# Performance work log

Measured on AMD Instinct MI355X. Metric: run time of the kernel, lower is better.

Reference implementation:

```python
import jax, jax.numpy as jnp
import numpy as np

TEMPERATURE = 0.07
EPS = 1e-8

def setup_inputs() -> dict:
    key = jax.random.key(0)
    k1, k2 = jax.random.split(key)
    features = jax.random.normal(k1, (8192, 512), dtype=jnp.float32)
    labels = jax.random.randint(k2, (8192,), 0, 100, dtype=jnp.int64)
    return {"features": features, "labels": labels}

def reference(features, labels):
    # L2-normalize rows (torch F.normalize uses eps=1e-12 clamp on norm)
    norm = jnp.maximum(jnp.linalg.norm(features, axis=1, keepdims=True), 1e-12)
    f = features / norm                                   # [B, D]
    sim = jnp.matmul(f, f.T) / TEMPERATURE                # [B, B]
    B = features.shape[0]
    same_label = (labels[:, None] == labels[None, :]).astype(features.dtype)
    diag = jnp.eye(B, dtype=bool)
    mask = jnp.where(diag, 0.0, same_label)               # positives, diag removed
    exp_sim = jnp.where(diag, 0.0, jnp.exp(sim))          # diag zeroed
    positive_sum = jnp.sum(exp_sim * mask, axis=1)        # [B]
    negative_sum = jnp.sum(exp_sim * (1.0 - mask), axis=1)
    loss = -jnp.log(positive_sum / (positive_sum + negative_sum + EPS))
    return loss.mean()
```

## Files before the change

kernel.cpp:

```cpp
#include <hip/hip_runtime.h>

#define BATCH 8192
#define DIM   512
#define NBLK  2080

typedef __attribute__((ext_vector_type(2))) long long2_t;
typedef __attribute__((ext_vector_type(4))) float f32x4;
typedef unsigned char u8;

__device__ __forceinline__ void gload_lds16(const void* g, void* l){
  __builtin_amdgcn_global_load_lds(
      (const __attribute__((address_space(1))) void*)g,
      (__attribute__((address_space(3))) void*)l, 16, 0, 0);
}

template<int CTRL>
__device__ __forceinline__ float dpp_add(float v){
  int s = __builtin_amdgcn_update_dpp(0, __float_as_int(v), CTRL, 0xF, 0xF, true);
  return v + __int_as_float(s);
}
__device__ __forceinline__ float red16(float v){
  v = dpp_add<0xB1>(v);
  v = dpp_add<0x4E>(v);
  v = dpp_add<0x141>(v);
  v = dpp_add<0x140>(v);
  return v;
}

__device__ __forceinline__ u8 f2e4m3(float v){
  unsigned s = (__float_as_uint(v) >> 24) & 0x80u;
  float a = fabsf(v);
  if (a < 0.0009765625f) return (u8)s;
  if (a < 0.015625f){
    int qd = (int)rintf(a * 512.0f);
    return (u8)(s | (unsigned)qd);
  }
  unsigned u = __float_as_uint(a);
  int E = (int)(u >> 23) - 127;
  unsigned m = u & 0x7FFFFF;
  unsigned mant = m >> 20;
  unsigned rem  = m & 0xFFFFF;
  mant += (rem > 0x80000u || (rem == 0x80000u && (mant & 1u))) ? 1u : 0u;
  if (mant == 8u){ mant = 0u; E += 1; }
  return (u8)(s | ((unsigned)(E + 7) << 3) | mant);
}

__global__ __launch_bounds__(256) void k_normalize(const float* __restrict__ x,
                                                   u8* __restrict__ q){
  const int row  = blockIdx.x * 4 + (threadIdx.x >> 6);
  const int lane = threadIdx.x & 63;
  const float* xr = x + (size_t)row * DIM + lane * 8;
  float4 a = *(const float4*)xr;
  float4 b = *(const float4*)(xr + 4);
  float s = a.x*a.x + a.y*a.y + a.z*a.z + a.w*a.w
          + b.x*b.x + b.y*b.y + b.z*b.z + b.w*b.w;
  #pragma unroll
  for (int m = 1; m < 64; m <<= 1) s += __shfl_xor(s, m);
  const float inv = 1.0f / fmaxf(sqrtf(s), 1e-12f);
  float f[8] = {a.x, a.y, a.z, a.w, b.x, b.y, b.z, b.w};
  union { u8 b[8]; unsigned long long u; } pk;
  #pragma unroll
  for (int e = 0; e < 8; e++) pk.b[e] = f2e4m3(f[e] * inv);
  const int kb = lane >> 3;
  const int g  = lane & 7;
  const int sw = (row >> 1) & 3;
  const size_t off = (size_t)row * DIM + kb * 64
                   + (size_t)(((g & 3) ^ sw) * 16 + (g >> 2) * 8);
  *(unsigned long long*)(q + off) = pk.u;
}

__global__ __launch_bounds__(256, 3) void k_gemm(const u8* __restrict__ q,
                                                 const int* __restrict__ labels,
                                                 float* __restrict__ ppos,
                                                 float* __restrict__ ptot){
  __shared__ u8 sA[2][128 * 64];
  __shared__ u8 sB[2][128 * 64];
  __shared__ int labI[128], labJ[128];

  const int bid = (blockIdx.x & 7) * 260 + (blockIdx.x >> 3);
  int bj = (int)((sqrtf(8.0f * (float)bid + 1.0f) - 1.0f) * 0.5f);
  while ((bj + 1) * (bj + 2) / 2 <= bid) bj++;
  while (bj * (bj + 1) / 2 > bid) bj--;
  const int bi = bid - bj * (bj + 1) / 2;
  const bool mirror = (bi != bj);
  const int rowbase = bi * 128, colbase = bj * 128;

  const int t    = threadIdx.x;
  const int lane = t & 63;
  const int w    = t >> 6;
  const int wr   = w >> 1, wc = w & 1;
  const int lrow = lane & 15;
  const int g    = lane >> 4;

  if (t < 128) labI[t] = labels[rowbase + t];
  else         labJ[t - 128] = labels[colbase + (t - 128)];

  const int gs = (g ^ ((lrow >> 1) & 3)) * 16;
  int ra[4], rb[4];
  #pragma unroll
  for (int m = 0; m < 4; m++) ra[m] = (wr * 64 + m * 16 + lrow) * 64 + gs;
  #pragma unroll
  for (int n = 0; n < 4; n++) rb[n] = (wc * 64 + n * 16 + lrow) * 64 + gs;

  const u8* srcA = q + (size_t)(rowbase + (t >> 2)) * DIM + (t & 3) * 16;
  const u8* srcB = q + (size_t)(colbase + (t >> 2)) * DIM + (t & 3) * 16;
  const int dL = t * 16;

#define STAGE(BUF, KT) do{                                                \
    gload_lds16(srcA + (KT) * 64,             sA[BUF] + dL);              \
    gload_lds16(srcA + (KT) * 64 + 64 * DIM,  sA[BUF] + dL + 4096);       \
    gload_lds16(srcB + (KT) * 64,             sB[BUF] + dL);              \
    gload_lds16(srcB + (KT) * 64 + 64 * DIM,  sB[BUF] + dL + 4096);       \
  }while(0)

  f32x4 acc[4][4];
  #pragma unroll
  for (int m = 0; m < 4; m++)
    #pragma unroll
    for (int n = 0; n < 4; n++)
      acc[m][n] = (f32x4){0.f, 0.f, 0.f, 0.f};

  STAGE(0, 0);
  __syncthreads();

  for (int kt = 0; kt < 8; ++kt){
    const int cur = kt & 1;
    if (kt < 7) STAGE(cur ^ 1, kt + 1);
    const u8* pA = sA[cur];
    const u8* pB = sB[cur];
    long2_t av[4], bv[4];
    #pragma unroll
    for (int n = 0; n < 4; n++) bv[n] = *(const long2_t*)(pB + rb[n]);
    #pragma unroll
    for (int m = 0; m < 4; m++) av[m] = *(const long2_t*)(pA + ra[m]);
    #pragma unroll
    for (int m = 0; m < 4; m++)
      #pragma unroll
      for (int n = 0; n < 4; n++)
        acc[m][n] = __builtin_amdgcn_mfma_f32_16x16x32_fp8_fp8(
            av[m][0], bv[n][0], acc[m][n], 0, 0, 0);
    #pragma unroll
    for (int m = 0; m < 4; m++)
      #pragma unroll
      for (int n = 0; n < 4; n++)
        acc[m][n] = __builtin_amdgcn_mfma_f32_16x16x32_fp8_fp8(
            av[m][1], bv[n][1], acc[m][n], 0, 0, 0);
    __syncthreads();
  }
#undef STAGE

  const int i0 = rowbase + wr * 64;
  const int j0 = colbase + wc * 64;

  int li_[4][4], lj_[4];
  #pragma unroll
  for (int m = 0; m < 4; m++)
    #pragma unroll
    for (int e = 0; e < 4; e++)
      li_[m][e] = labI[wr * 64 + m * 16 + g * 4 + e];
  #pragma unroll
  for (int n = 0; n < 4; n++)
    lj_[n] = labJ[wc * 64 + n * 16 + lrow];

  const float invT = 14.285714285714286f;
  #pragma unroll
  for (int m = 0; m < 4; m++)
    #pragma unroll
    for (int n = 0; n < 4; n++)
      #pragma unroll
      for (int e = 0; e < 4; e++){
        int i = i0 + m * 16 + g * 4 + e;
        int j = j0 + n * 16 + lrow;
        acc[m][n][e] = (i == j) ? 0.0f : __expf(acc[m][n][e] * invT);
      }

  {
    float* pp = ppos + (size_t)(2 * bj + wc) * BATCH;
    float* pt = ptot + (size_t)(2 * bj + wc) * BATCH;
    #pragma unroll
    for (int m = 0; m < 4; m++){
      float tr[4] = {0, 0, 0, 0}, pr[4] = {0, 0, 0, 0};
      #pragma unroll
      for (int n = 0; n < 4; n++){
        int lj = lj_[n];
        #pragma unroll
        for (int e = 0; e < 4; e++){
          float v = acc[m][n][e];
          tr[e] += v;
          pr[e] += (li_[m][e] == lj) ? v : 0.0f;
        }
      }
      #pragma unroll
      for (int e = 0; e < 4; e++){
        tr[e] = red16(tr[e]);
        pr[e] = red16(pr[e]);
      }
      if (lrow == 0){
        int ib = i0 + m * 16 + g * 4;
        #pragma unroll
        for (int e = 0; e < 4; e++){
          pt[ib + e] = tr[e];
          pp[ib + e] = pr[e];
        }
      }
    }
  }

  if (mirror){
    float* pp = ppos + (size_t)(2 * bi + wr) * BATCH;
    float* pt = ptot + (size_t)(2 * bi + wr) * BATCH;
    #pragma unroll
    for (int n = 0; n < 4; n++){
      float ts = 0.f, ps = 0.f;
      int lj = lj_[n];
      #pragma unroll
      for (int m = 0; m < 4; m++)
        #pragma unroll
        for (int e = 0; e < 4; e++){
          float v = acc[m][n][e];
          ts += v;
          ps += (li_[m][e] == lj) ? v : 0.0f;
        }
      ts += __shfl_xor(ts, 16); ps += __shfl_xor(ps, 16);
      ts += __shfl_xor(ts, 32); ps += __shfl_xor(ps, 32);
      if (lane < 16){
        int j = j0 + n * 16 + lane;
        pt[j] = ts;
        pp[j] = ps;
      }
    }
  }
}

__global__ __launch_bounds__(256) void k_rowloss(const float* __restrict__ ppos,
                                                 const float* __restrict__ ptot,
                                                 float* __restrict__ bsum){
  __shared__ float sp[256], st2[256];
  const int t = threadIdx.x;
  const int r = blockIdx.x * 32 + (t & 31);
  const int c0 = t >> 5;
  float p = 0.f, tt = 0.f;
  for (int c = c0; c < 128; c += 8){
    p  += ppos[(size_t)c * BATCH + r];
    tt += ptot[(size_t)c * BATCH + r];
  }
  sp[t] = p; st2[t] = tt;
  __syncthreads();
  if (t < 32){
    float P = 0.f, T = 0.f;
    #pragma unroll
    for (int k = 0; k < 8; k++){ P += sp[t + k * 32]; T += st2[t + k * 32]; }
    sp[t] = -logf(P / (T + 1e-8f));
  }
  __syncthreads();
  if (t == 0){
    float s = 0.f;
    #pragma unroll
    for (int k = 0; k < 32; k++) s += sp[k];
    bsum[blockIdx.x] = s;
  }
}

__global__ __launch_bounds__(256) void k_final(const float* __restrict__ bsum,
                                               float* __restrict__ out){
  __shared__ float s4[4];
  float v = bsum[threadIdx.x];
  #pragma unroll
  for (int m = 1; m < 64; m <<= 1) v += __shfl_xor(v, m);
  if ((threadIdx.x & 63) == 0) s4[threadIdx.x >> 6] = v;
  __syncthreads();
  if (threadIdx.x == 0) out[0] = (s4[0] + s4[1] + s4[2] + s4[3]) * (1.0f / 8192.0f);
}

extern "C" void kernel_launch(void* const* d_in, const int* in_sizes, int n_in,
                              void* d_out, int out_size, void* d_ws, size_t ws_size,
                              hipStream_t stream){
  const float* x      = (const float*)d_in[0];
  const int*   labels = (const int*)d_in[1];
  float*       out    = (float*)d_out;

  char* ws = (char*)d_ws;
  u8*    q    = (u8*)ws;
  float* ppos = (float*)(ws + 8388608);
  float* ptot = (float*)(ws + 8388608 + 4194304);
  float* bsum = (float*)(ws + 8388608 + 8388608);

  k_normalize<<<BATCH / 4, 256, 0, stream>>>(x, q);
  k_gemm<<<NBLK, 256, 8192, stream>>>(q, labels, ppos, ptot);
  k_rowloss<<<256, 256, 0, stream>>>(ppos, ptot, bsum);
  k_final<<<1, 256, 0, stream>>>(bsum, out);
}
```

Before: 56.15 us.

## Convert triangular GEMM to persistent kernel with atomic tile scheduler

```diff
diff --git a/kernel.cpp b/kernel.cpp
--- a/kernel.cpp
+++ b/kernel.cpp
@@ -2,7 +2,8 @@
 
 #define BATCH 8192
 #define DIM   512
-#define NBLK  2080
+#define NTILE 2080
+#define GRID  768
 
 typedef __attribute__((ext_vector_type(2))) long long2_t;
 typedef __attribute__((ext_vector_type(4))) float f32x4;
@@ -46,7 +47,9 @@
 }
 
 __global__ __launch_bounds__(256) void k_normalize(const float* __restrict__ x,
-                                                   u8* __restrict__ q){
+                                                   u8* __restrict__ q,
+                                                   int* __restrict__ counter){
+  if (blockIdx.x == 0 && threadIdx.x == 0) counter[0] = 0;
   const int row  = blockIdx.x * 4 + (threadIdx.x >> 6);
   const int lane = threadIdx.x & 63;
   const float* xr = x + (size_t)row * DIM + lane * 8;
@@ -72,18 +75,12 @@
 __global__ __launch_bounds__(256, 3) void k_gemm(const u8* __restrict__ q,
                                                  const int* __restrict__ labels,
                                                  float* __restrict__ ppos,
-                                                 float* __restrict__ ptot){
+                                                 float* __restrict__ ptot,
+                                                 int* __restrict__ counter){
   __shared__ u8 sA[2][128 * 64];
   __shared__ u8 sB[2][128 * 64];
   __shared__ int labI[128], labJ[128];
-
-  const int bid = (blockIdx.x & 7) * 260 + (blockIdx.x >> 3);
-  int bj = (int)((sqrtf(8.0f * (float)bid + 1.0f) - 1.0f) * 0.5f);
-  while ((bj + 1) * (bj + 2) / 2 <= bid) bj++;
-  while (bj * (bj + 1) / 2 > bid) bj--;
-  const int bi = bid - bj * (bj + 1) / 2;
-  const bool mirror = (bi != bj);
-  const int rowbase = bi * 128, colbase = bj * 128;
+  __shared__ int sTile;
 
   const int t    = threadIdx.x;
   const int lane = t & 63;
@@ -92,19 +89,32 @@
   const int lrow = lane & 15;
   const int g    = lane >> 4;
 
-  if (t < 128) labI[t] = labels[rowbase + t];
-  else         labJ[t - 128] = labels[colbase + (t - 128)];
-
   const int gs = (g ^ ((lrow >> 1) & 3)) * 16;
   int ra[4], rb[4];
   #pragma unroll
   for (int m = 0; m < 4; m++) ra[m] = (wr * 64 + m * 16 + lrow) * 64 + gs;
   #pragma unroll
   for (int n = 0; n < 4; n++) rb[n] = (wc * 64 + n * 16 + lrow) * 64 + gs;
-
-  const u8* srcA = q + (size_t)(rowbase + (t >> 2)) * DIM + (t & 3) * 16;
-  const u8* srcB = q + (size_t)(colbase + (t >> 2)) * DIM + (t & 3) * 16;
   const int dL = t * 16;
+
+  for (;;){
+    if (t == 0) sTile = atomicAdd(counter, 1);
+    __syncthreads();
+    const int bid = sTile;
+    if (bid >= NTILE) break;
+
+    int bj = (int)((sqrtf(8.0f * (float)bid + 1.0f) - 1.0f) * 0.5f);
+    while ((bj + 1) * (bj + 2) / 2 <= bid) bj++;
+    while (bj * (bj + 1) / 2 > bid) bj--;
+    const int bi = bid - bj * (bj + 1) / 2;
+    const bool mirror = (bi != bj);
+    const int rowbase = bi * 128, colbase = bj * 128;
+
+    if (t < 128) labI[t] = labels[rowbase + t];
+    else         labJ[t - 128] = labels[colbase + (t - 128)];
+
+    const u8* srcA = q + (size_t)(rowbase + (t >> 2)) * DIM + (t & 3) * 16;
+    const u8* srcB = q + (size_t)(colbase + (t >> 2)) * DIM + (t & 3) * 16;
 
 #define STAGE(BUF, KT) do{                                                \
     gload_lds16(srcA + (KT) * 64,             sA[BUF] + dL);              \
@@ -113,120 +123,123 @@
     gload_lds16(srcB + (KT) * 64 + 64 * DIM,  sB[BUF] + dL + 4096);       \
   }while(0)
 
-  f32x4 acc[4][4];
-  #pragma unroll
-  for (int m = 0; m < 4; m++)
+    f32x4 acc[4][4];
+    #pragma unroll
+    for (int m = 0; m < 4; m++)
+      #pragma unroll
+      for (int n = 0; n < 4; n++)
+        acc[m][n] = (f32x4){0.f, 0.f, 0.f, 0.f};
+
+    STAGE(0, 0);
+    __syncthreads();
+
+    for (int kt = 0; kt < 8; ++kt){
+      const int cur = kt & 1;
+      if (kt < 7) STAGE(cur ^ 1, kt + 1);
+      const u8* pA = sA[cur];
+      const u8* pB = sB[cur];
+      long2_t av[4], bv[4];
+      #pragma unroll
+      for (int n = 0; n < 4; n++) bv[n] = *(const long2_t*)(pB + rb[n]);
+      #pragma unroll
+      for (int m = 0; m < 4; m++) av[m] = *(const long2_t*)(pA + ra[m]);
+      #pragma unroll
+      for (int m = 0; m < 4; m++)
+        #pragma unroll
+        for (int n = 0; n < 4; n++)
+          acc[m][n] = __builtin_amdgcn_mfma_f32_16x16x32_fp8_fp8(
+              av[m][0], bv[n][0], acc[m][n], 0, 0, 0);
+      #pragma unroll
+      for (int m = 0; m < 4; m++)
+        #pragma unroll
+        for (int n = 0; n < 4; n++)
+          acc[m][n] = __builtin_amdgcn_mfma_f32_16x16x32_fp8_fp8(
+              av[m][1], bv[n][1], acc[m][n], 0, 0, 0);
+      __syncthreads();
+    }
+#undef STAGE
+
+    const int i0 = rowbase + wr * 64;
+    const int j0 = colbase + wc * 64;
+
+    int lj_[4];
     #pragma unroll
     for (int n = 0; n < 4; n++)
-      acc[m][n] = (f32x4){0.f, 0.f, 0.f, 0.f};
-
-  STAGE(0, 0);
-  __syncthreads();
-
-  for (int kt = 0; kt < 8; ++kt){
-    const int cur = kt & 1;
-    if (kt < 7) STAGE(cur ^ 1, kt + 1);
-    const u8* pA = sA[cur];
-    const u8* pB = sB[cur];
-    long2_t av[4], bv[4];
-    #pragma unroll
-    for (int n = 0; n < 4; n++) bv[n] = *(const long2_t*)(pB + rb[n]);
-    #pragma unroll
-    for (int m = 0; m < 4; m++) av[m] = *(const long2_t*)(pA + ra[m]);
+      lj_[n] = labJ[wc * 64 + n * 16 + lrow];
+
+    const float invT = 14.285714285714286f;
     #pragma unroll
     for (int m = 0; m < 4; m++)
       #pragma unroll
       for (int n = 0; n < 4; n++)
-        acc[m][n] = __builtin_amdgcn_mfma_f32_16x16x32_fp8_fp8(
-            av[m][0], bv[n][0], acc[m][n], 0, 0, 0);
-    #pragma unroll
-    for (int m = 0; m < 4; m++)
-      #pragma unroll
-      for (int n = 0; n < 4; n++)
-        acc[m][n] = __builtin_amdgcn_mfma_f32_16x16x32_fp8_fp8(
-            av[m][1], bv[n][1], acc[m][n], 0, 0, 0);
-    __syncthreads();
-  }
-#undef STAGE
-
-  const int i0 = rowbase + wr * 64;
-  const int j0 = colbase + wc * 64;
-
-  int li_[4][4], lj_[4];
-  #pragma unroll
-  for (int m = 0; m < 4; m++)
-    #pragma unroll
-    for (int e = 0; e < 4; e++)
-      li_[m][e] = labI[wr * 64 + m * 16 + g * 4 + e];
-  #pragma unroll
-  for (int n = 0; n < 4; n++)
-    lj_[n] = labJ[wc * 64 + n * 16 + lrow];
-
-  const float invT = 14.285714285714286f;
-  #pragma unroll
-  for (int m = 0; m < 4; m++)
-    #pragma unroll
-    for (int n = 0; n < 4; n++)
-      #pragma unroll
-      for (int e = 0; e < 4; e++){
-        int i = i0 + m * 16 + g * 4 + e;
-        int j = j0 + n * 16 + lrow;
-        acc[m][n][e] = (i == j) ? 0.0f : __expf(acc[m][n][e] * invT);
-      }
-
-  {
-    float* pp = ppos + (size_t)(2 * bj + wc) * BATCH;
-    float* pt = ptot + (size_t)(2 * bj + wc) * BATCH;
-    #pragma unroll
-    for (int m = 0; m < 4; m++){
-      float tr[4] = {0, 0, 0, 0}, pr[4] = {0, 0, 0, 0};
-      #pragma unroll
-      for (int n = 0; n < 4; n++){
-        int lj = lj_[n];
         #pragma unroll
         for (int e = 0; e < 4; e++){
-          float v = acc[m][n][e];
-          tr[e] += v;
-          pr[e] += (li_[m][e] == lj) ? v : 0.0f;
-        }
-      }
-      #pragma unroll
-      for (int e = 0; e < 4; e++){
-        tr[e] = red16(tr[e]);
-        pr[e] = red16(pr[e]);
-      }
-      if (lrow == 0){
-        int ib = i0 + m * 16 + g * 4;
+          int i = i0 + m * 16 + g * 4 + e;
+          int j = j0 + n * 16 + lrow;
+          acc[m][n][e] = (i == j) ? 0.0f : __expf(acc[m][n][e] * invT);
+        }
+
+    {
+      float* pp = ppos + (size_t)(2 * bj + wc) * BATCH;
+      float* pt = ptot + (size_t)(2 * bj + wc) * BATCH;
+      #pragma unroll
+      for (int m = 0; m < 4; m++){
+        int li4[4];
+        #pragma unroll
+        for (int e = 0; e < 4; e++) li4[e] = labI[wr * 64 + m * 16 + g * 4 + e];
+        float tr[4] = {0, 0, 0, 0}, pr[4] = {0, 0, 0, 0};
+        #pragma unroll
+        for (int n = 0; n < 4; n++){
+          int lj = lj_[n];
+          #pragma unroll
+          for (int e = 0; e < 4; e++){
+            float v = acc[m][n][e];
+            tr[e] += v;
+            pr[e] += (li4[e] == lj) ? v : 0.0f;
+          }
+        }
         #pragma unroll
         for (int e = 0; e < 4; e++){
-          pt[ib + e] = tr[e];
-          pp[ib + e] = pr[e];
+          tr[e] = red16(tr[e]);
+          pr[e] = red16(pr[e]);
+        }
+        if (lrow == 0){
+          int ib = i0 + m * 16 + g * 4;
+          #pragma unroll
+          for (int e = 0; e < 4; e++){
+            pt[ib + e] = tr[e];
+            pp[ib + e] = pr[e];
+          }
         }
       }
     }
-  }
-
-  if (mirror){
-    float* pp = ppos + (size_t)(2 * bi + wr) * BATCH;
-    float* pt = ptot + (size_t)(2 * bi + wr) * BATCH;
-    #pragma unroll
-    for (int n = 0; n < 4; n++){
-      float ts = 0.f, ps = 0.f;
-      int lj = lj_[n];
-      #pragma unroll
-      for (int m = 0; m < 4; m++)
-        #pragma unroll
-        for (int e = 0; e < 4; e++){
-          float v = acc[m][n][e];
-          ts += v;
-          ps += (li_[m][e] == lj) ? v : 0.0f;
-        }
-      ts += __shfl_xor(ts, 16); ps += __shfl_xor(ps, 16);
-      ts += __shfl_xor(ts, 32); ps += __shfl_xor(ps, 32);
-      if (lane < 16){
-        int j = j0 + n * 16 + lane;
-        pt[j] = ts;
-        pp[j] = ps;
+
+    if (mirror){
+      float* pp = ppos + (size_t)(2 * bi + wr) * BATCH;
+      float* pt = ptot + (size_t)(2 * bi + wr) * BATCH;
+      #pragma unroll
+      for (int n = 0; n < 4; n++){
+        float ts = 0.f, ps = 0.f;
+        int lj = lj_[n];
+        #pragma unroll
+        for (int m = 0; m < 4; m++){
+          int li4[4];
+          #pragma unroll
+          for (int e = 0; e < 4; e++) li4[e] = labI[wr * 64 + m * 16 + g * 4 + e];
+          #pragma unroll
+          for (int e = 0; e < 4; e++){
+            float v = acc[m][n][e];
+            ts += v;
+            ps += (li4[e] == lj) ? v : 0.0f;
+          }
+        }
+        ts += __shfl_xor(ts, 16); ps += __shfl_xor(ps, 16);
+        ts += __shfl_xor(ts, 32); ps += __shfl_xor(ps, 32);
+        if (lane < 16){
+          int j = j0 + n * 16 + lane;
+          pt[j] = ts;
+          pp[j] = ps;
+        }
       }
     }
   }
@@ -284,9 +297,10 @@
   float* ppos = (float*)(ws + 8388608);
   float* ptot = (float*)(ws + 8388608 + 4194304);
   float* bsum = (float*)(ws + 8388608 + 8388608);
-
-  k_normalize<<<BATCH / 4, 256, 0, stream>>>(x, q);
-  k_gemm<<<NBLK, 256, 8192, stream>>>(q, labels, ppos, ptot);
+  int*   cnt  = (int*)(ws + 8388608 + 8388608 + 1024);
+
+  k_normalize<<<BATCH / 4, 256, 0, stream>>>(x, q, cnt);
+  k_gemm<<<GRID, 256, 0, stream>>>(q, labels, ppos, ptot, cnt);
   k_rowloss<<<256, 256, 0, stream>>>(ppos, ptot, bsum);
   k_final<<<1, 256, 0, stream>>>(bsum, out);
 }
```

New measurement: 70.85 us. 1.26x slower.
